# Kernel tuning notes

Hardware: AMD Instinct MI355X
Metric: run time of the kernel (lower is better)

The kernel has to match this reference:

```python
import jax, jax.numpy as jnp
import numpy as np

M = 512; N = 512; H = 1.0; DX = 1.0; DY = 1.0
NUM_ITERS = 600            # enough Jacobi iterations for the wavefront to cross a 512x512 grid
Q = 4000000                # num_event * num_station query points
INF = 1e5                  # 'infinity' initialization for travel times


def eikonal_solve(f_flat, m1, n1):
    """Parallel (Jacobi) fast-iterative Eikonal solve |grad u| = f on an MxN grid,
    Godunov upwind update, source at (m1, n1). Converges to the same viscosity
    solution as the original C++ fast-sweeping kernel."""
    f = f_flat.reshape(M, N)
    fh = f * H
    u0 = jnp.full((M, N), INF, dtype=f_flat.dtype).at[m1, n1].set(0.0)

    def step(u, _):
        up = jnp.pad(u, 1, constant_values=INF)
        a = jnp.minimum(up[:-2, 1:-1], up[2:, 1:-1])   # min over x-neighbors
        b = jnp.minimum(up[1:-1, :-2], up[1:-1, 2:])   # min over y-neighbors
        one_sided = jnp.minimum(a, b) + fh
        disc = 2.0 * fh * fh - (a - b) ** 2
        two_sided = 0.5 * (a + b + jnp.sqrt(jnp.maximum(disc, 0.0)))
        u_new = jnp.where(jnp.abs(a - b) >= fh, one_sided, two_sided)
        u = jnp.minimum(u, u_new).at[m1, n1].set(0.0)
        return u, None

    u, _ = jax.lax.scan(step, u0, None, length=NUM_ITERS)
    return u.reshape(-1)


def bilinear(u, gridx, gridy):
    """Faithful translation of the module's gather-based bilinear interpolation,
    including the original's quirks (f_x2y1 used for both w12 and w21 terms,
    f_x1y2 computed but unused)."""
    xu = jnp.ceil(gridx); xl = jnp.floor(gridx)
    yu = jnp.ceil(gridy); yl = jnp.floor(gridy)
    g_uu = (xu * N + yu).astype(jnp.int32)
    g_ul = (xu * N + yl).astype(jnp.int32)
    g_lu = (xl * N + yu).astype(jnp.int32)
    g_ll = (xl * N + yl).astype(jnp.int32)
    f_x2y2 = u[g_uu]
    f_x2y1 = u[g_ul]
    f_x1y1 = u[g_ll]
    f_x1y2 = u[g_lu]  # computed but unused, as in the source
    xh = xu - gridx; xlw = gridx - xl
    yh = yu - gridy; ylw = gridy - yl
    w11 = xh * yh; w12 = xh * ylw; w21 = xlw * yh; w22 = xlw * ylw
    return (w11 * f_x1y1 + w12 * f_x2y1 + w21 * f_x2y1 + w22 * f_x2y2) * (1.0 / (DX * DY))


def setup_inputs() -> dict:
    key = jax.random.key(0)
    kf, kx, ky = jax.random.split(key, 3)
    f = 0.5 + jax.random.uniform(kf, (M * N,), jnp.float32)           # slowness field ~U[0.5,1.5]
    gridx = jax.random.uniform(kx, (Q,), jnp.float32) * (M - 2)       # query x in [0, M-2]
    gridy = jax.random.uniform(ky, (Q,), jnp.float32) * (N - 2)       # query y in [0, N-2]
    return {"f": f, "gridx": gridx, "gridy": gridy, "m1": 256, "n1": 256}


def reference(f, gridx, gridy, m1, n1):
    u = eikonal_solve(f, m1, n1)
    return bilinear(u, gridx, gridy)
```

## Files before the change

kernel.cpp:

```cpp
#include <hip/hip_runtime.h>

#define M_    512
#define N_    512
#define INF_  1e5f
#define FBIG  1e30f
#define TR    16
#define TC    32
#define K_    24
#define TWR   64
#define TWC   80
#define SD    88
#define QPR   20
#define NQ    (62*QPR)
#define NT    1024

#if !__has_builtin(__builtin_amdgcn_sqrtf)
#define __builtin_amdgcn_sqrtf sqrtf
#endif

__device__ __forceinline__ float cell_upd(float xn0, float xn1, float yn0, float yn1,
                                          float uc, float fh, float t2) {
    float a   = fminf(xn0, xn1);
    float b   = fminf(yn0, yn1);
    float amb = a - b;
    float one = fminf(a, b) + fh;
    float dis = fmaf(-amb, amb, t2);
    float two = 0.5f * (a + b + __builtin_amdgcn_sqrtf(fmaxf(dis, 0.0f)));
    float un  = (fabsf(amb) >= fh) ? one : two;
    return fminf(uc, un);
}

__device__ __forceinline__ void quad_update(const float* __restrict__ cur,
                                            float* __restrict__ nxt, int off4,
                                            const float* __restrict__ fq,
                                            const float* __restrict__ tq) {
    const int off = off4 * 4;
    float4 up = *(const float4*)(cur + off - SD);
    float4 dn = *(const float4*)(cur + off + SD);
    float4 ct = *(const float4*)(cur + off);
    float  lf = cur[off - 1];
    float  rt = cur[off + 4];
    float4 o;
    o.x = cell_upd(up.x, dn.x, lf,   ct.y, ct.x, fq[0], tq[0]);
    o.y = cell_upd(up.y, dn.y, ct.x, ct.z, ct.y, fq[1], tq[1]);
    o.z = cell_upd(up.z, dn.z, ct.y, ct.w, ct.z, fq[2], tq[2]);
    o.w = cell_upd(up.w, dn.w, ct.z, rt,   ct.w, fq[3], tq[3]);
    *(float4*)(nxt + off) = o;
}

__global__ __launch_bounds__(NT) void jacobi_k(const float* __restrict__ u_in,
                                               float* __restrict__ u_out,
                                               const float* __restrict__ f,
                                               const int* __restrict__ m1p,
                                               const int* __restrict__ n1p,
                                               int first) {
    __shared__ float sA[TWR * SD];
    __shared__ float sB[TWR * SD];
    const int tid = threadIdx.x;
    const int bx  = blockIdx.x & 15;
    const int by  = blockIdx.x >> 4;
    const int gr0 = by * TR - K_;
    const int gc0 = bx * TC - K_;
    const int srcR = m1p[0], srcC = n1p[0];

    for (int idx = tid; idx < TWR * TWC; idx += NT) {
        int r = idx / TWC, c = idx - r * TWC;
        int gr = gr0 + r, gc = gc0 + c;
        float uv = INF_;
        if (first) {
            uv = (gr == srcR && gc == srcC) ? 0.0f : INF_;
        } else if ((unsigned)gr < (unsigned)M_ && (unsigned)gc < (unsigned)N_) {
            uv = u_in[(gr << 9) + gc];
        }
        sA[r * SD + c + 3] = uv;
    }

    int off0, off1 = 0, life0, life1 = 0;
    float fq0[4], tq0[4], fq1[4], tq1[4];
    {
        int qr = tid / QPR, qk = tid - qr * QPR;
        int r0 = qr + 1, c0 = 1 + 4 * qk;
        off0  = 22 * r0 + 1 + qk;
        life0 = min(min(r0, 63 - r0), min(c0 + 3, 79 - c0));
        #pragma unroll
        for (int j = 0; j < 4; ++j) {
            int gr = gr0 + r0, gc = gc0 + c0 + j;
            float fv = FBIG;
            if ((unsigned)gr < (unsigned)M_ && (unsigned)gc < (unsigned)N_)
                fv = f[(gr << 9) + gc];
            fq0[j] = fv; tq0[j] = 2.0f * fv * fv;
        }
    }
    if (tid + NT < NQ) {
        int qi = tid + NT;
        int qr = qi / QPR, qk = qi - qr * QPR;
        int r1 = qr + 1, c1 = 1 + 4 * qk;
        off1  = 22 * r1 + 1 + qk;
        life1 = min(min(r1, 63 - r1), min(c1 + 3, 79 - c1));
        #pragma unroll
        for (int j = 0; j < 4; ++j) {
            int gr = gr0 + r1, gc = gc0 + c1 + j;
            float fv = FBIG;
            if ((unsigned)gr < (unsigned)M_ && (unsigned)gc < (unsigned)N_)
                fv = f[(gr << 9) + gc];
            fq1[j] = fv; tq1[j] = 2.0f * fv * fv;
        }
    }
    __syncthreads();

    float* cur = sA;
    float* nxt = sB;
    for (int t = 0; t < K_; ++t) {
        if (t < life0) quad_update(cur, nxt, off0, fq0, tq0);
        if (t < life1) quad_update(cur, nxt, off1, fq1, tq1);
        __syncthreads();
        float* tmp = cur; cur = nxt; nxt = tmp;
    }

    if (tid < TR * TC) {
        int r = tid >> 5, c = tid & 31;
        u_out[((by * TR + r) << 9) + bx * TC + c] = cur[(K_ + r) * SD + (K_ + 3 + c)];
    }
}

__device__ __forceinline__ float bil1(const float* __restrict__ u, float gx, float gy) {
    float xu = ceilf(gx),  xl = floorf(gx);
    float yu = ceilf(gy),  yl = floorf(gy);
    int guu = (int)(xu * (float)N_ + yu);
    int gul = (int)(xu * (float)N_ + yl);
    int gll = (int)(xl * (float)N_ + yl);
    float f22 = u[guu];
    float f21 = u[gul];
    float f11 = u[gll];
    float xh = xu - gx, xlw = gx - xl;
    float yh = yu - gy, ylw = gy - yl;
    float w11 = xh * yh, w12 = xh * ylw, w21 = xlw * yh, w22 = xlw * ylw;
    return w11 * f11 + w12 * f21 + w21 * f21 + w22 * f22;
}

__global__ __launch_bounds__(256) void bilin(const float* __restrict__ u,
                                             const float* __restrict__ gx,
                                             const float* __restrict__ gy,
                                             float* __restrict__ out, int q4) {
    int i = blockIdx.x * blockDim.x + threadIdx.x;
    int stride = gridDim.x * blockDim.x;
    for (; i < q4; i += stride) {
        float4 x = reinterpret_cast<const float4*>(gx)[i];
        float4 y = reinterpret_cast<const float4*>(gy)[i];
        float4 o;
        o.x = bil1(u, x.x, y.x);
        o.y = bil1(u, x.y, y.y);
        o.z = bil1(u, x.z, y.z);
        o.w = bil1(u, x.w, y.w);
        reinterpret_cast<float4*>(out)[i] = o;
    }
}

extern "C" void kernel_launch(void* const* d_in, const int* in_sizes, int n_in,
                              void* d_out, int out_size, void* d_ws, size_t ws_size,
                              hipStream_t stream) {
    const float* f  = (const float*)d_in[0];
    const float* gx = (const float*)d_in[1];
    const float* gy = (const float*)d_in[2];
    const int*   m1 = (const int*)d_in[3];
    const int*   n1 = (const int*)d_in[4];
    float* out = (float*)d_out;

    float* ua = (float*)d_ws;
    float* ub = ua + M_ * N_;
    const int Q = in_sizes[1];

    const float* src = ub;
    float*       dst = ua;
    for (int l = 0; l < 25; ++l) {
        jacobi_k<<<512, NT, 0, stream>>>(src, dst, f, m1, n1, l == 0 ? 1 : 0);
        float* t = (float*)src; src = dst; dst = t;
    }

    bilin<<<4096, 256, 0, stream>>>(src, gx, gy, out, Q / 4);
}
```

Before: 867.2 us.

## Replace block barriers with neighbor-wave flag sync and enlarge tiles to 32x32

Each block's output tile grows from 16x32 to 32x32 over an 80x80 shared window, so the launch uses 256 blocks and less of the work goes to redundant halo cells. Each wave now owns a band of rows. The per-step __syncthreads is replaced by LDS flags: a wave only waits for its two neighboring waves to finish the previous step. The center quad is also carried in registers across steps instead of being re-read from LDS. The cost is spin-wait overhead, a dependence on correct LDS memory ordering through volatile flags, and only one large block per CU.

```diff
diff --git a/kernel.cpp b/kernel.cpp
--- a/kernel.cpp
+++ b/kernel.cpp
@@ -4,15 +4,13 @@
 #define N_    512
 #define INF_  1e5f
 #define FBIG  1e30f
-#define TR    16
-#define TC    32
+#define T_    32
 #define K_    24
-#define TWR   64
-#define TWC   80
+#define TW    80
 #define SD    88
 #define QPR   20
-#define NQ    (62*QPR)
 #define NT    1024
+#define NW    16
 
 #if !__has_builtin(__builtin_amdgcn_sqrtf)
 #define __builtin_amdgcn_sqrtf sqrtf
@@ -30,14 +28,12 @@
     return fminf(uc, un);
 }
 
-__device__ __forceinline__ void quad_update(const float* __restrict__ cur,
-                                            float* __restrict__ nxt, int off4,
+__device__ __forceinline__ float4 quad_step(const float* __restrict__ cur, float4 ct, int off4,
                                             const float* __restrict__ fq,
                                             const float* __restrict__ tq) {
     const int off = off4 * 4;
     float4 up = *(const float4*)(cur + off - SD);
     float4 dn = *(const float4*)(cur + off + SD);
-    float4 ct = *(const float4*)(cur + off);
     float  lf = cur[off - 1];
     float  rt = cur[off + 4];
     float4 o;
@@ -45,7 +41,7 @@
     o.y = cell_upd(up.y, dn.y, ct.x, ct.z, ct.y, fq[1], tq[1]);
     o.z = cell_upd(up.z, dn.z, ct.y, ct.w, ct.z, fq[2], tq[2]);
     o.w = cell_upd(up.w, dn.w, ct.z, rt,   ct.w, fq[3], tq[3]);
-    *(float4*)(nxt + off) = o;
+    return o;
 }
 
 __global__ __launch_bounds__(NT) void jacobi_k(const float* __restrict__ u_in,
@@ -54,17 +50,22 @@
                                                const int* __restrict__ m1p,
                                                const int* __restrict__ n1p,
                                                int first) {
-    __shared__ float sA[TWR * SD];
-    __shared__ float sB[TWR * SD];
-    const int tid = threadIdx.x;
-    const int bx  = blockIdx.x & 15;
-    const int by  = blockIdx.x >> 4;
-    const int gr0 = by * TR - K_;
-    const int gc0 = bx * TC - K_;
+    __shared__ float sA[TW * SD];
+    __shared__ float sB[TW * SD];
+    __shared__ int   flags[NW];
+    const int tid  = threadIdx.x;
+    const int lane = tid & 63;
+    const int w    = tid >> 6;
+    const int bx   = blockIdx.x & 15;
+    const int by   = blockIdx.x >> 4;
+    const int gr0  = by * T_ - K_;
+    const int gc0  = bx * T_ - K_;
     const int srcR = m1p[0], srcC = n1p[0];
 
-    for (int idx = tid; idx < TWR * TWC; idx += NT) {
-        int r = idx / TWC, c = idx - r * TWC;
+    if (tid < NW) flags[tid] = 0;
+
+    for (int idx = tid; idx < TW * TW; idx += NT) {
+        int r = idx / TW, c = idx - r * TW;
         int gr = gr0 + r, gc = gc0 + c;
         float uv = INF_;
         if (first) {
@@ -75,31 +76,31 @@
         sA[r * SD + c + 3] = uv;
     }
 
-    int off0, off1 = 0, life0, life1 = 0;
+    const int rlo = 1 + 5 * w;
+    const int nq  = (w < 15) ? 100 : 60;
+    int off0 = 0, life0 = 0, off1 = 0, life1 = 0;
     float fq0[4], tq0[4], fq1[4], tq1[4];
-    {
-        int qr = tid / QPR, qk = tid - qr * QPR;
-        int r0 = qr + 1, c0 = 1 + 4 * qk;
-        off0  = 22 * r0 + 1 + qk;
-        life0 = min(min(r0, 63 - r0), min(c0 + 3, 79 - c0));
+    if (lane < nq) {
+        int r = rlo + lane / QPR, qk = lane % QPR, c = 1 + 4 * qk;
+        off0  = 22 * r + 1 + qk;
+        life0 = min(min(r, 79 - r), min(c + 3, 79 - c));
         #pragma unroll
         for (int j = 0; j < 4; ++j) {
-            int gr = gr0 + r0, gc = gc0 + c0 + j;
+            int gr = gr0 + r, gc = gc0 + c + j;
             float fv = FBIG;
             if ((unsigned)gr < (unsigned)M_ && (unsigned)gc < (unsigned)N_)
                 fv = f[(gr << 9) + gc];
             fq0[j] = fv; tq0[j] = 2.0f * fv * fv;
         }
     }
-    if (tid + NT < NQ) {
-        int qi = tid + NT;
-        int qr = qi / QPR, qk = qi - qr * QPR;
-        int r1 = qr + 1, c1 = 1 + 4 * qk;
-        off1  = 22 * r1 + 1 + qk;
-        life1 = min(min(r1, 63 - r1), min(c1 + 3, 79 - c1));
+    if (w < 15 && lane < 36) {
+        int q = lane + 64;
+        int r = rlo + q / QPR, qk = q % QPR, c = 1 + 4 * qk;
+        off1  = 22 * r + 1 + qk;
+        life1 = min(min(r, 79 - r), min(c + 3, 79 - c));
         #pragma unroll
         for (int j = 0; j < 4; ++j) {
-            int gr = gr0 + r1, gc = gc0 + c1 + j;
+            int gr = gr0 + r, gc = gc0 + c + j;
             float fv = FBIG;
             if ((unsigned)gr < (unsigned)M_ && (unsigned)gc < (unsigned)N_)
                 fv = f[(gr << 9) + gc];
@@ -108,18 +109,29 @@
     }
     __syncthreads();
 
-    float* cur = sA;
-    float* nxt = sB;
+    float4 ct0 = *(const float4*)(sA + off0 * 4);
+    float4 ct1 = *(const float4*)(sA + off1 * 4);
+
+    volatile int* vf = flags;
+    const float* cur = sA;
+    float*       nxt = sB;
     for (int t = 0; t < K_; ++t) {
-        if (t < life0) quad_update(cur, nxt, off0, fq0, tq0);
-        if (t < life1) quad_update(cur, nxt, off1, fq1, tq1);
-        __syncthreads();
-        float* tmp = cur; cur = nxt; nxt = tmp;
+        if (t) {
+            if (w > 0)      while (vf[w - 1] < t) __builtin_amdgcn_s_sleep(1);
+            if (w < NW - 1) while (vf[w + 1] < t) __builtin_amdgcn_s_sleep(1);
+            asm volatile("" ::: "memory");
+        }
+        if (t < life0) { ct0 = quad_step(cur, ct0, off0, fq0, tq0); *(float4*)(nxt + off0 * 4) = ct0; }
+        if (t < life1) { ct1 = quad_step(cur, ct1, off1, fq1, tq1); *(float4*)(nxt + off1 * 4) = ct1; }
+        asm volatile("s_waitcnt lgkmcnt(0)" ::: "memory");
+        if (lane == 0) vf[w] = t + 1;
+        const float* tmp = cur; cur = nxt; nxt = (float*)tmp;
     }
 
-    if (tid < TR * TC) {
+    __syncthreads();
+    {
         int r = tid >> 5, c = tid & 31;
-        u_out[((by * TR + r) << 9) + bx * TC + c] = cur[(K_ + r) * SD + (K_ + 3 + c)];
+        u_out[((by * T_ + r) << 9) + bx * T_ + c] = cur[(K_ + r) * SD + (K_ + 3 + c)];
     }
 }
 
@@ -173,7 +185,7 @@
     const float* src = ub;
     float*       dst = ua;
     for (int l = 0; l < 25; ++l) {
-        jacobi_k<<<512, NT, 0, stream>>>(src, dst, f, m1, n1, l == 0 ? 1 : 0);
+        jacobi_k<<<256, NT, 0, stream>>>(src, dst, f, m1, n1, l == 0 ? 1 : 0);
         float* t = (float*)src; src = dst; dst = t;
     }
 
```

After: 856.0 us. About the same (-1.3%).
